# Performance work log

Hardware: AMD Instinct MI355X
Metric: run time of the kernel (lower is better)

Reference implementation:

```python
import jax, jax.numpy as jnp
import numpy as np

C = 512
H = 8
P = 64
B = 4
N = 1024


def setup_inputs() -> dict:
    key = jax.random.key(0)
    ks = jax.random.split(key, 12)
    s = 0.02
    return {
        "tokens": jax.random.normal(ks[0], (B, N, C), dtype=jnp.float32),
        "pair_features": jax.random.normal(ks[1], (N, N, P), dtype=jnp.float32),
        "Wq": jax.random.normal(ks[2], (C, C), dtype=jnp.float32) * s,
        "bq": jnp.zeros((C,), dtype=jnp.float32),
        "Wk": jax.random.normal(ks[3], (C, C), dtype=jnp.float32) * s,
        "bk": jnp.zeros((C,), dtype=jnp.float32),
        "Wv": jax.random.normal(ks[4], (C, C), dtype=jnp.float32) * s,
        "bv": jnp.zeros((C,), dtype=jnp.float32),
        "Wo": jax.random.normal(ks[5], (C, C), dtype=jnp.float32) * s,
        "bo": jnp.zeros((C,), dtype=jnp.float32),
        "Wp": jax.random.normal(ks[6], (P, H), dtype=jnp.float32) * s,
    }


def reference(tokens, pair_features, Wq, bq, Wk, bk, Wv, bv, Wo, bo, Wp):
    b, n, c = tokens.shape
    h = H
    d = c // h
    scale = d ** -0.5
    # projections -> [b, h, n, d]
    q = (tokens @ Wq + bq).reshape(b, n, h, d).transpose(0, 2, 1, 3)
    k = (tokens @ Wk + bk).reshape(b, n, h, d).transpose(0, 2, 1, 3)
    v = (tokens @ Wv + bv).reshape(b, n, h, d).transpose(0, 2, 1, 3)
    # attention logits [b, h, n, n] with additive pair-derived bias [h, n, n]
    logits = jnp.einsum('bhnd,bhmd->bhnm', q, k) * scale
    pair_bias = jnp.einsum('nmp,ph->hnm', pair_features, Wp)
    logits = logits + pair_bias[None]
    attn = jax.nn.softmax(logits, axis=-1)  # dropout p=0.0 -> identity
    merged = jnp.einsum('bhnm,bhmd->bhnd', attn, v)
    merged = merged.transpose(0, 2, 1, 3).reshape(b, n, c)
    return merged @ Wo + bo
```

## Files before the change

kernel.cpp:

```cpp
#include <hip/hip_runtime.h>
#include <hip/hip_bf16.h>
#include <stdint.h>
#include <stddef.h>

typedef __bf16 bf16x8 __attribute__((ext_vector_type(8)));
typedef __bf16 bf16x4 __attribute__((ext_vector_type(4)));
typedef float  f32x4  __attribute__((ext_vector_type(4)));
typedef uint32_t __attribute__((address_space(3))) lds_u32;
typedef uint32_t __attribute__((address_space(1))) glob_u32;

#define PAIR_BLOCKS 2048
#define CAST_BLOCKS 2048
#define TR_BLOCKS   256
#define NSPLIT 2
#define NITER  8
#define LOG2E 1.4426950408889634f

__global__ __launch_bounds__(256) void prep_kernel(
    const float* __restrict__ tokens, const float* __restrict__ pf,
    const float* __restrict__ Wq, const float* __restrict__ Wk,
    const float* __restrict__ Wv, const float* __restrict__ Wo,
    const float* __restrict__ Wp,
    __bf16* __restrict__ tok_bf, __bf16* __restrict__ WcatT,
    __bf16* __restrict__ WoT, __bf16* __restrict__ pbb) {
  __shared__ float ls[64][65];
  int bx = blockIdx.x, tid = threadIdx.x;
  if (bx < PAIR_BLOCKS) {
    int wave = tid >> 6, lane = tid & 63;
    int lg = lane >> 4, lr = lane & 15;
    bf16x8 whi[2], wlo[2];
#pragma unroll
    for (int s = 0; s < 2; ++s)
#pragma unroll
      for (int j = 0; j < 8; ++j) {
        int p = s * 32 + lg * 8 + j;
        float w = (lr < 8) ? Wp[p * 8 + lr] : 0.f;
        __bf16 h = (__bf16)w;
        whi[s][j] = h;
        wlo[s][j] = (__bf16)(w - (float)h);
      }
    int wbase = bx * 512 + wave * 128;
#pragma unroll 2
    for (int t = 0; t < 8; ++t) {
      int rowt = wbase + t * 16;
      const float* rp = pf + (size_t)(rowt + lr) * 64;
      f32x4 raw[2][2];
#pragma unroll
      for (int s = 0; s < 2; ++s) {
        raw[s][0] = *(const f32x4*)&rp[s * 32 + lg * 8];
        raw[s][1] = *(const f32x4*)&rp[s * 32 + lg * 8 + 4];
      }
      bf16x8 ahi[2], alo[2];
#pragma unroll
      for (int s = 0; s < 2; ++s)
#pragma unroll
        for (int j = 0; j < 8; ++j) {
          float x = raw[s][j >> 2][j & 3];
          __bf16 h = (__bf16)x;
          ahi[s][j] = h;
          alo[s][j] = (__bf16)(x - (float)h);
        }
      f32x4 acc = {0.f, 0.f, 0.f, 0.f};
#pragma unroll
      for (int s = 0; s < 2; ++s) {
        acc = __builtin_amdgcn_mfma_f32_16x16x32_bf16(ahi[s], whi[s], acc, 0, 0, 0);
        acc = __builtin_amdgcn_mfma_f32_16x16x32_bf16(ahi[s], wlo[s], acc, 0, 0, 0);
        acc = __builtin_amdgcn_mfma_f32_16x16x32_bf16(alo[s], whi[s], acc, 0, 0, 0);
      }
      if (lr < 8) {
        bf16x4 pk;
#pragma unroll
        for (int r = 0; r < 4; ++r) pk[r] = (__bf16)(acc[r] * LOG2E);
        *(bf16x4*)&pbb[((size_t)lr << 20) + rowt + lg * 4] = pk;
      }
    }
  } else if (bx < PAIR_BLOCKS + CAST_BLOCKS) {
    int i = (bx - PAIR_BLOCKS) * 256 + tid;
    float4 f = ((const float4*)tokens)[i];
    bf16x4 v;
    v[0] = (__bf16)f.x; v[1] = (__bf16)f.y; v[2] = (__bf16)f.z; v[3] = (__bf16)f.w;
    ((bf16x4*)tok_bf)[i] = v;
  } else {
    int t = bx - (PAIR_BLOCKS + CAST_BLOCKS);
    int which = t >> 6; t &= 63;
    const float* in = which == 0 ? Wq : which == 1 ? Wk : which == 2 ? Wv : Wo;
    __bf16* out = which < 3 ? (WcatT + (size_t)which * 512 * 512) : WoT;
    int tc = (t & 7) * 64, tr = (t >> 3) * 64;
#pragma unroll
    for (int i = 0; i < 16; ++i) {
      int e = tid + i * 256, r = e >> 6, c = e & 63;
      ls[r][c] = in[(size_t)(tr + r) * 512 + tc + c];
    }
    __syncthreads();
#pragma unroll
    for (int i = 0; i < 16; ++i) {
      int e = tid + i * 256, r = e >> 6, c = e & 63;
      out[(size_t)(tc + r) * 512 + tr + c] = (__bf16)ls[c][r];
    }
  }
}

__device__ __forceinline__ void gemm_mainloop_128(const __bf16* __restrict__ A,
                                                  const __bf16* __restrict__ Bt,
                                                  int K, int m0, int n0,
                                                  f32x4 (&acc)[4][4]) {
  __shared__ __bf16 As[128][40];
  __shared__ __bf16 Bs[128][40];
  int tid = threadIdx.x;
  int wave = tid >> 6, lane = tid & 63;
  int wm = (wave >> 1) * 64, wn = (wave & 1) * 64;
  int lg = lane >> 4, lr = lane & 15;
#pragma unroll
  for (int i = 0; i < 4; ++i)
#pragma unroll
    for (int j = 0; j < 4; ++j) acc[i][j] = (f32x4){0.f, 0.f, 0.f, 0.f};

  for (int k0 = 0; k0 < K; k0 += 32) {
    __syncthreads();
#pragma unroll
    for (int i = 0; i < 2; ++i) {
      int cid = tid + i * 256;
      int row = cid >> 2, c8 = (cid & 3) * 8;
      *(bf16x8*)&As[row][c8] = *(const bf16x8*)&A[(size_t)(m0 + row) * K + k0 + c8];
      *(bf16x8*)&Bs[row][c8] = *(const bf16x8*)&Bt[(size_t)(n0 + row) * K + k0 + c8];
    }
    __syncthreads();
    bf16x8 af[4], bfr[4];
#pragma unroll
    for (int i = 0; i < 4; ++i) {
      af[i]  = *(const bf16x8*)&As[wm + i * 16 + lr][lg * 8];
      bfr[i] = *(const bf16x8*)&Bs[wn + i * 16 + lr][lg * 8];
    }
#pragma unroll
    for (int i = 0; i < 4; ++i)
#pragma unroll
      for (int j = 0; j < 4; ++j)
        acc[i][j] = __builtin_amdgcn_mfma_f32_16x16x32_bf16(af[i], bfr[j], acc[i][j], 0, 0, 0);
  }
}

__global__ __launch_bounds__(256) void qkv_gemm_kernel(const __bf16* __restrict__ A,
                                                       const __bf16* __restrict__ Bt,
                                                       const float* __restrict__ bq,
                                                       const float* __restrict__ bk,
                                                       const float* __restrict__ bv,
                                                       __bf16* __restrict__ qb,
                                                       __bf16* __restrict__ kb,
                                                       __bf16* __restrict__ vtb) {
  const float qscale = 0.125f * LOG2E;
  int m0 = blockIdx.y * 128, n0 = blockIdx.x * 128;
  f32x4 acc[4][4];
  gemm_mainloop_128(A, Bt, 512, m0, n0, acc);
  int tid = threadIdx.x, wave = tid >> 6, lane = tid & 63;
  int wm = (wave >> 1) * 64, wn = (wave & 1) * 64, lg = lane >> 4, lr = lane & 15;
#pragma unroll
  for (int i = 0; i < 4; ++i)
#pragma unroll
    for (int j = 0; j < 4; ++j) {
      int grow0 = m0 + wm + i * 16 + lg * 4;
      int gcol = n0 + wn + j * 16 + lr;
      int sel = gcol >> 9, c = gcol & 511;
      int hh = c >> 6, dd = c & 63;
      int b = grow0 >> 10, n = grow0 & 1023;
      if (sel == 2) {
        float bias = bv[c];
        bf16x4 pack;
#pragma unroll
        for (int r = 0; r < 4; ++r) pack[r] = (__bf16)(acc[i][j][r] + bias);
        *(bf16x4*)&vtb[(((size_t)(b * 8 + hh)) * 64 + dd) * 1024 + n] = pack;
      } else if (sel == 0) {
        float bias = bq[c];
#pragma unroll
        for (int r = 0; r < 4; ++r)
          qb[(((size_t)(b * 8 + hh)) * 1024 + n + r) * 64 + dd] = (__bf16)((acc[i][j][r] + bias) * qscale);
      } else {
        float bias = bk[c];
#pragma unroll
        for (int r = 0; r < 4; ++r)
          kb[(((size_t)(b * 8 + hh)) * 1024 + n + r) * 64 + dd] = (__bf16)(acc[i][j][r] + bias);
      }
    }
}

__device__ __forceinline__ bf16x8 swz_read(const __bf16* buf, int r, int k) {
  int chunk = (r << 3) | (k ^ (r & 7));
  return *(const bf16x8*)&buf[chunk * 8];
}

__global__ __launch_bounds__(256) void flash_kernel(const __bf16* __restrict__ qg,
                                                    const __bf16* __restrict__ kg,
                                                    const __bf16* __restrict__ vtg,
                                                    const __bf16* __restrict__ pbg,
                                                    float* __restrict__ po,
                                                    float2* __restrict__ ml) {
  __shared__ __align__(16) __bf16 kvs[2][2][64 * 64];
  __shared__ __bf16 pls[4][16][72];
  int bh = blockIdx.y, z = blockIdx.z, h = bh & 7;
  int q0 = blockIdx.x * 64;
  int tid = threadIdx.x, wave = tid >> 6, lane = tid & 63;
  int lg = lane >> 4, lr = lane & 15;
  const __bf16* qp = qg + (size_t)bh * 65536;
  const __bf16* kp = kg + (size_t)bh * 65536;
  const __bf16* vp = vtg + (size_t)bh * 65536;
  const __bf16* pbh = pbg + ((size_t)h << 20);
  int qw0 = q0 + wave * 16;
  int kb0 = z * NITER;

  auto stage = [&](int buf, int kb2) {
#pragma unroll
    for (int p = 0; p < 2; ++p) {
      int c = p * 256 + wave * 64 + lane;
      int r = c >> 3, kk = c & 7;
      int g = (c & ~7) | (kk ^ (r & 7));
      const __bf16* gk = kp + (size_t)kb2 * 4096 + g * 8;
      const __bf16* gv = vp + (size_t)(g >> 3) * 1024 + kb2 * 64 + (g & 7) * 8;
      __builtin_amdgcn_global_load_lds((const glob_u32*)gk,
          (lds_u32*)&kvs[buf][0][(size_t)(p * 256 + wave * 64) * 8], 16, 0, 0);
      __builtin_amdgcn_global_load_lds((const glob_u32*)gv,
          (lds_u32*)&kvs[buf][1][(size_t)(p * 256 + wave * 64) * 8], 16, 0, 0);
    }
  };

  bf16x8 qf[2];
#pragma unroll
  for (int c = 0; c < 2; ++c)
    qf[c] = *(const bf16x8*)&qp[(size_t)(qw0 + lr) * 64 + c * 32 + lg * 8];

  float mrow = -1e30f, lrow = 0.f;
  f32x4 of[4] = {};

  stage(0, kb0);
  __syncthreads();

#pragma unroll
  for (int t = 0; t < NITER; ++t) {
    int kb2 = kb0 + t;
    if (t + 1 < NITER) stage((t + 1) & 1, kb2 + 1);
    const __bf16* kbuf = &kvs[t & 1][0][0];
    const __bf16* vbuf = &kvs[t & 1][1][0];

    bf16x8 kf[4][2];
#pragma unroll
    for (int n = 0; n < 4; ++n)
#pragma unroll
      for (int c = 0; c < 2; ++c)
        kf[n][c] = swz_read(kbuf, n * 16 + lr, c * 4 + lg);

    f32x4 sv[4];
#pragma unroll
    for (int n = 0; n < 4; ++n) {
      bf16x4 bias = *(const bf16x4*)&pbh[(size_t)(qw0 + lr) * 1024 + kb2 * 64 + n * 16 + lg * 4];
      f32x4 cb;
#pragma unroll
      for (int r = 0; r < 4; ++r) cb[r] = (float)bias[r];
      cb = __builtin_amdgcn_mfma_f32_16x16x32_bf16(kf[n][0], qf[0], cb, 0, 0, 0);
      cb = __builtin_amdgcn_mfma_f32_16x16x32_bf16(kf[n][1], qf[1], cb, 0, 0, 0);
      sv[n] = cb;
    }

    float tm = -1e30f;
#pragma unroll
    for (int n = 0; n < 4; ++n)
#pragma unroll
      for (int r = 0; r < 4; ++r) tm = fmaxf(tm, sv[n][r]);
    tm = fmaxf(tm, __shfl_xor(tm, 16));
    tm = fmaxf(tm, __shfl_xor(tm, 32));
    float newm = fmaxf(mrow, tm);
    float fs = exp2f(mrow - newm);
    mrow = newm;
    float rs = 0.f;
#pragma unroll
    for (int n = 0; n < 4; ++n)
#pragma unroll
      for (int r = 0; r < 4; ++r) {
        float p = exp2f(sv[n][r] - newm);
        sv[n][r] = p;
        rs += p;
      }
    rs += __shfl_xor(rs, 16);
    rs += __shfl_xor(rs, 32);
    lrow = lrow * fs + rs;

#pragma unroll
    for (int n = 0; n < 4; ++n) {
      bf16x4 pk;
#pragma unroll
      for (int r = 0; r < 4; ++r) pk[r] = (__bf16)sv[n][r];
      *(bf16x4*)&pls[wave][lr][n * 16 + lg * 4] = pk;
    }

#pragma unroll
    for (int r = 0; r < 4; ++r) {
      float fsq = __shfl(fs, (lane & 48) | (lg * 4 + r));
#pragma unroll
      for (int dn = 0; dn < 4; ++dn) of[dn][r] *= fsq;
    }

    bf16x8 pa[2];
#pragma unroll
    for (int c = 0; c < 2; ++c)
      pa[c] = *(const bf16x8*)&pls[wave][lr][c * 32 + lg * 8];
    bf16x8 vf[4][2];
#pragma unroll
    for (int dn = 0; dn < 4; ++dn)
#pragma unroll
      for (int c = 0; c < 2; ++c)
        vf[dn][c] = swz_read(vbuf, dn * 16 + lr, c * 4 + lg);
#pragma unroll
    for (int dn = 0; dn < 4; ++dn) {
      of[dn] = __builtin_amdgcn_mfma_f32_16x16x32_bf16(pa[0], vf[dn][0], of[dn], 0, 0, 0);
      of[dn] = __builtin_amdgcn_mfma_f32_16x16x32_bf16(pa[1], vf[dn][1], of[dn], 0, 0, 0);
    }
    __syncthreads();
  }

  if (lg == 0)
    ml[(size_t)z * 32768 + bh * 1024 + qw0 + lr] = make_float2(mrow, lrow);
#pragma unroll
  for (int r = 0; r < 4; ++r) {
    int q = qw0 + lg * 4 + r;
#pragma unroll
    for (int dn = 0; dn < 4; ++dn)
      po[((size_t)z * 32768 + bh * 1024 + q) * 64 + dn * 16 + lr] = of[dn][r];
  }
}

__global__ __launch_bounds__(256) void combine_kernel(const float* __restrict__ po,
                                                      const float2* __restrict__ ml,
                                                      __bf16* __restrict__ merged) {
  int e = blockIdx.x * 256 + threadIdx.x;
  int row = e >> 5, d2 = (e & 31) * 2;
  int bh = row >> 10, q = row & 1023, b = bh >> 3, h = bh & 7;
  float2 s[NSPLIT];
  float M = -1e30f;
#pragma unroll
  for (int zz = 0; zz < NSPLIT; ++zz) {
    s[zz] = ml[(size_t)zz * 32768 + row];
    M = fmaxf(M, s[zz].x);
  }
  float L = 0.f, ox = 0.f, oy = 0.f;
#pragma unroll
  for (int zz = 0; zz < NSPLIT; ++zz) {
    float w = exp2f(s[zz].x - M);
    L += w * s[zz].y;
    float2 p = *(const float2*)&po[((size_t)zz * 32768 + row) * 64 + d2];
    ox += w * p.x;
    oy += w * p.y;
  }
  float inv = 1.f / L;
  __bf16 pr[2] = {(__bf16)(ox * inv), (__bf16)(oy * inv)};
  *(uint32_t*)&merged[((size_t)(b * 1024 + q)) * 512 + h * 64 + d2] = *(uint32_t*)pr;
}

__global__ __launch_bounds__(256) void out_gemm_kernel(const __bf16* __restrict__ A,
                                                       const __bf16* __restrict__ Bt,
                                                       const float* __restrict__ bo,
                                                       float* __restrict__ out) {
  int m0 = blockIdx.y * 128, n0 = blockIdx.x * 128;
  f32x4 acc[4][4];
  gemm_mainloop_128(A, Bt, 512, m0, n0, acc);
  int tid = threadIdx.x, wave = tid >> 6, lane = tid & 63;
  int wm = (wave >> 1) * 64, wn = (wave & 1) * 64, lg = lane >> 4, lr = lane & 15;
#pragma unroll
  for (int i = 0; i < 4; ++i)
#pragma unroll
    for (int j = 0; j < 4; ++j)
#pragma unroll
      for (int r = 0; r < 4; ++r) {
        int grow = m0 + wm + i * 16 + lg * 4 + r;
        int gcol = n0 + wn + j * 16 + lr;
        out[(size_t)grow * 512 + gcol] = acc[i][j][r] + bo[gcol];
      }
}

extern "C" void kernel_launch(void* const* d_in, const int* in_sizes, int n_in,
                              void* d_out, int out_size, void* d_ws, size_t ws_size,
                              hipStream_t stream) {
  const float* tokens = (const float*)d_in[0];
  const float* pf     = (const float*)d_in[1];
  const float* Wq     = (const float*)d_in[2];
  const float* bq     = (const float*)d_in[3];
  const float* Wk     = (const float*)d_in[4];
  const float* bk     = (const float*)d_in[5];
  const float* Wv     = (const float*)d_in[6];
  const float* bv     = (const float*)d_in[7];
  const float* Wo     = (const float*)d_in[8];
  const float* bo     = (const float*)d_in[9];
  const float* Wp     = (const float*)d_in[10];
  float* out = (float*)d_out;

  char* ws = (char*)d_ws;
  size_t off = 0;
  auto alloc = [&](size_t bytes) { char* p = ws + off; off += (bytes + 255) & ~(size_t)255; return p; };
  __bf16* tok_bf = (__bf16*)alloc((size_t)4096 * 512 * 2);
  __bf16* WcatT  = (__bf16*)alloc((size_t)1536 * 512 * 2);
  __bf16* WoT    = (__bf16*)alloc((size_t)512 * 512 * 2);
  __bf16* qb     = (__bf16*)alloc((size_t)32 * 1024 * 64 * 2);
  __bf16* kb     = (__bf16*)alloc((size_t)32 * 1024 * 64 * 2);
  __bf16* vtb    = (__bf16*)alloc((size_t)32 * 64 * 1024 * 2);
  __bf16* pbb    = (__bf16*)alloc((size_t)8 * 1024 * 1024 * 2);
  __bf16* merged = (__bf16*)alloc((size_t)4096 * 512 * 2);
  float*  po     = (float*)alloc((size_t)NSPLIT * 32 * 1024 * 64 * 4);
  float2* ml     = (float2*)alloc((size_t)NSPLIT * 32 * 1024 * 8);

  prep_kernel<<<PAIR_BLOCKS + CAST_BLOCKS + TR_BLOCKS, 256, 0, stream>>>(
      tokens, pf, Wq, Wk, Wv, Wo, Wp, tok_bf, WcatT, WoT, pbb);
  qkv_gemm_kernel<<<dim3(12, 32), 256, 0, stream>>>(tok_bf, WcatT, bq, bk, bv, qb, kb, vtb);
  flash_kernel<<<dim3(16, 32, NSPLIT), 256, 0, stream>>>(qb, kb, vtb, pbb, po, ml);
  combine_kernel<<<4096, 256, 0, stream>>>(po, ml, merged);
  out_gemm_kernel<<<dim3(4, 32), 256, 0, stream>>>(merged, WoT, bo, out);
}
```

Baseline: 142.5 us.

## Fuse weight cast into GEMMs, merge prep with QKV, fold split combine into flash

The separate token/weight bf16 cast and transpose pass is removed. The QKV and output GEMMs now load fp32 tokens and weights directly and convert and transpose them in LDS. The QKV GEMM runs as extra blocks inside the pair-bias prep kernel, and the split-K combine is done by whichever flash block finishes last for each tile, using an atomic counter. This cuts the launch count from five to three and avoids workspace round-trips, at the cost of redundant fp32 weight conversion per block, more LDS per block, and a reliance on threadfence/atomic ordering.

```diff
diff --git a/kernel.cpp b/kernel.cpp
--- a/kernel.cpp
+++ b/kernel.cpp
@@ -9,23 +9,113 @@
 typedef uint32_t __attribute__((address_space(3))) lds_u32;
 typedef uint32_t __attribute__((address_space(1))) glob_u32;
 
+#define QKV_BLOCKS 384
 #define PAIR_BLOCKS 2048
-#define CAST_BLOCKS 2048
-#define TR_BLOCKS   256
+#define FLAG_BLOCKS 2
 #define NSPLIT 2
 #define NITER  8
 #define LOG2E 1.4426950408889634f
 
-__global__ __launch_bounds__(256) void prep_kernel(
+__global__ __launch_bounds__(256) void k1_kernel(
     const float* __restrict__ tokens, const float* __restrict__ pf,
     const float* __restrict__ Wq, const float* __restrict__ Wk,
-    const float* __restrict__ Wv, const float* __restrict__ Wo,
-    const float* __restrict__ Wp,
-    __bf16* __restrict__ tok_bf, __bf16* __restrict__ WcatT,
-    __bf16* __restrict__ WoT, __bf16* __restrict__ pbb) {
-  __shared__ float ls[64][65];
+    const float* __restrict__ Wv, const float* __restrict__ Wp,
+    const float* __restrict__ bq, const float* __restrict__ bk,
+    const float* __restrict__ bv,
+    __bf16* __restrict__ qb, __bf16* __restrict__ kb, __bf16* __restrict__ vtb,
+    __bf16* __restrict__ pbb, int* __restrict__ flag) {
+  __shared__ __bf16 As[128][40];
+  __shared__ __bf16 Bs[128][40];
+  __shared__ float ftile[32][133];
   int bx = blockIdx.x, tid = threadIdx.x;
-  if (bx < PAIR_BLOCKS) {
+  if (bx < QKV_BLOCKS) {
+    const float qscale = 0.125f * LOG2E;
+    int nb = bx % 12, mb = bx / 12;
+    int m0 = mb * 128, n0 = nb * 128;
+    int sel = n0 >> 9, cloc = n0 & 511;
+    const float* W = sel == 0 ? Wq : sel == 1 ? Wk : Wv;
+    int wave = tid >> 6, lane = tid & 63;
+    int wm = (wave >> 1) * 64, wn = (wave & 1) * 64;
+    int lg = lane >> 4, lr = lane & 15;
+    f32x4 acc[4][4];
+#pragma unroll
+    for (int i = 0; i < 4; ++i)
+#pragma unroll
+      for (int j = 0; j < 4; ++j) acc[i][j] = (f32x4){0.f, 0.f, 0.f, 0.f};
+
+    for (int k0 = 0; k0 < 512; k0 += 32) {
+      __syncthreads();
+#pragma unroll
+      for (int i = 0; i < 2; ++i) {
+        int cid = tid + i * 256;
+        int row = cid >> 2, c8 = (cid & 3) * 8;
+        const float* src = &tokens[(size_t)(m0 + row) * 512 + k0 + c8];
+        f32x4 f0 = *(const f32x4*)src, f1 = *(const f32x4*)(src + 4);
+        bf16x8 v;
+#pragma unroll
+        for (int u = 0; u < 4; ++u) { v[u] = (__bf16)f0[u]; v[u + 4] = (__bf16)f1[u]; }
+        *(bf16x8*)&As[row][c8] = v;
+      }
+#pragma unroll
+      for (int i = 0; i < 2; ++i) {
+        int cid = tid + i * 256;
+        int kk = cid >> 4, n8 = (cid & 15) * 8;
+        const float* src = &W[(size_t)(k0 + kk) * 512 + cloc + n8];
+        *(f32x4*)&ftile[kk][n8] = *(const f32x4*)src;
+        *(f32x4*)&ftile[kk][n8 + 4] = *(const f32x4*)(src + 4);
+      }
+      __syncthreads();
+#pragma unroll
+      for (int i = 0; i < 2; ++i) {
+        int cid = tid + i * 256;
+        int n = cid >> 2, kk8 = (cid & 3) * 8;
+        bf16x8 v;
+#pragma unroll
+        for (int u = 0; u < 8; ++u) v[u] = (__bf16)ftile[kk8 + u][n];
+        *(bf16x8*)&Bs[n][kk8] = v;
+      }
+      __syncthreads();
+      bf16x8 af[4], bfr[4];
+#pragma unroll
+      for (int i = 0; i < 4; ++i) {
+        af[i]  = *(const bf16x8*)&As[wm + i * 16 + lr][lg * 8];
+        bfr[i] = *(const bf16x8*)&Bs[wn + i * 16 + lr][lg * 8];
+      }
+#pragma unroll
+      for (int i = 0; i < 4; ++i)
+#pragma unroll
+        for (int j = 0; j < 4; ++j)
+          acc[i][j] = __builtin_amdgcn_mfma_f32_16x16x32_bf16(af[i], bfr[j], acc[i][j], 0, 0, 0);
+    }
+#pragma unroll
+    for (int i = 0; i < 4; ++i)
+#pragma unroll
+      for (int j = 0; j < 4; ++j) {
+        int grow0 = m0 + wm + i * 16 + lg * 4;
+        int gcol = n0 + wn + j * 16 + lr;
+        int gsel = gcol >> 9, c = gcol & 511;
+        int hh = c >> 6, dd = c & 63;
+        int b = grow0 >> 10, n = grow0 & 1023;
+        if (gsel == 2) {
+          float bias = bv[c];
+          bf16x4 pack;
+#pragma unroll
+          for (int r = 0; r < 4; ++r) pack[r] = (__bf16)(acc[i][j][r] + bias);
+          *(bf16x4*)&vtb[(((size_t)(b * 8 + hh)) * 64 + dd) * 1024 + n] = pack;
+        } else if (gsel == 0) {
+          float bias = bq[c];
+#pragma unroll
+          for (int r = 0; r < 4; ++r)
+            qb[(((size_t)(b * 8 + hh)) * 1024 + n + r) * 64 + dd] = (__bf16)((acc[i][j][r] + bias) * qscale);
+        } else {
+          float bias = bk[c];
+#pragma unroll
+          for (int r = 0; r < 4; ++r)
+            kb[(((size_t)(b * 8 + hh)) * 1024 + n + r) * 64 + dd] = (__bf16)(acc[i][j][r] + bias);
+        }
+      }
+  } else if (bx < QKV_BLOCKS + PAIR_BLOCKS) {
+    int pb = bx - QKV_BLOCKS;
     int wave = tid >> 6, lane = tid & 63;
     int lg = lane >> 4, lr = lane & 15;
     bf16x8 whi[2], wlo[2];
@@ -39,7 +129,7 @@
         whi[s][j] = h;
         wlo[s][j] = (__bf16)(w - (float)h);
       }
-    int wbase = bx * 512 + wave * 128;
+    int wbase = pb * 512 + wave * 128;
 #pragma unroll 2
     for (int t = 0; t < 8; ++t) {
       int rowt = wbase + t * 16;
@@ -74,112 +164,10 @@
         *(bf16x4*)&pbb[((size_t)lr << 20) + rowt + lg * 4] = pk;
       }
     }
-  } else if (bx < PAIR_BLOCKS + CAST_BLOCKS) {
-    int i = (bx - PAIR_BLOCKS) * 256 + tid;
-    float4 f = ((const float4*)tokens)[i];
-    bf16x4 v;
-    v[0] = (__bf16)f.x; v[1] = (__bf16)f.y; v[2] = (__bf16)f.z; v[3] = (__bf16)f.w;
-    ((bf16x4*)tok_bf)[i] = v;
   } else {
-    int t = bx - (PAIR_BLOCKS + CAST_BLOCKS);
-    int which = t >> 6; t &= 63;
-    const float* in = which == 0 ? Wq : which == 1 ? Wk : which == 2 ? Wv : Wo;
-    __bf16* out = which < 3 ? (WcatT + (size_t)which * 512 * 512) : WoT;
-    int tc = (t & 7) * 64, tr = (t >> 3) * 64;
-#pragma unroll
-    for (int i = 0; i < 16; ++i) {
-      int e = tid + i * 256, r = e >> 6, c = e & 63;
-      ls[r][c] = in[(size_t)(tr + r) * 512 + tc + c];
-    }
-    __syncthreads();
-#pragma unroll
-    for (int i = 0; i < 16; ++i) {
-      int e = tid + i * 256, r = e >> 6, c = e & 63;
-      out[(size_t)(tc + r) * 512 + tr + c] = (__bf16)ls[c][r];
-    }
-  }
-}
-
-__device__ __forceinline__ void gemm_mainloop_128(const __bf16* __restrict__ A,
-                                                  const __bf16* __restrict__ Bt,
-                                                  int K, int m0, int n0,
-                                                  f32x4 (&acc)[4][4]) {
-  __shared__ __bf16 As[128][40];
-  __shared__ __bf16 Bs[128][40];
-  int tid = threadIdx.x;
-  int wave = tid >> 6, lane = tid & 63;
-  int wm = (wave >> 1) * 64, wn = (wave & 1) * 64;
-  int lg = lane >> 4, lr = lane & 15;
-#pragma unroll
-  for (int i = 0; i < 4; ++i)
-#pragma unroll
-    for (int j = 0; j < 4; ++j) acc[i][j] = (f32x4){0.f, 0.f, 0.f, 0.f};
-
-  for (int k0 = 0; k0 < K; k0 += 32) {
-    __syncthreads();
-#pragma unroll
-    for (int i = 0; i < 2; ++i) {
-      int cid = tid + i * 256;
-      int row = cid >> 2, c8 = (cid & 3) * 8;
-      *(bf16x8*)&As[row][c8] = *(const bf16x8*)&A[(size_t)(m0 + row) * K + k0 + c8];
-      *(bf16x8*)&Bs[row][c8] = *(const bf16x8*)&Bt[(size_t)(n0 + row) * K + k0 + c8];
-    }
-    __syncthreads();
-    bf16x8 af[4], bfr[4];
-#pragma unroll
-    for (int i = 0; i < 4; ++i) {
-      af[i]  = *(const bf16x8*)&As[wm + i * 16 + lr][lg * 8];
-      bfr[i] = *(const bf16x8*)&Bs[wn + i * 16 + lr][lg * 8];
-    }
-#pragma unroll
-    for (int i = 0; i < 4; ++i)
-#pragma unroll
-      for (int j = 0; j < 4; ++j)
-        acc[i][j] = __builtin_amdgcn_mfma_f32_16x16x32_bf16(af[i], bfr[j], acc[i][j], 0, 0, 0);
-  }
-}
-
-__global__ __launch_bounds__(256) void qkv_gemm_kernel(const __bf16* __restrict__ A,
-                                                       const __bf16* __restrict__ Bt,
-                                                       const float* __restrict__ bq,
-                                                       const float* __restrict__ bk,
-                                                       const float* __restrict__ bv,
-                                                       __bf16* __restrict__ qb,
-                                                       __bf16* __restrict__ kb,
-                                                       __bf16* __restrict__ vtb) {
-  const float qscale = 0.125f * LOG2E;
-  int m0 = blockIdx.y * 128, n0 = blockIdx.x * 128;
-  f32x4 acc[4][4];
-  gemm_mainloop_128(A, Bt, 512, m0, n0, acc);
-  int tid = threadIdx.x, wave = tid >> 6, lane = tid & 63;
-  int wm = (wave >> 1) * 64, wn = (wave & 1) * 64, lg = lane >> 4, lr = lane & 15;
-#pragma unroll
-  for (int i = 0; i < 4; ++i)
-#pragma unroll
-    for (int j = 0; j < 4; ++j) {
-      int grow0 = m0 + wm + i * 16 + lg * 4;
-      int gcol = n0 + wn + j * 16 + lr;
-      int sel = gcol >> 9, c = gcol & 511;
-      int hh = c >> 6, dd = c & 63;
-      int b = grow0 >> 10, n = grow0 & 1023;
-      if (sel == 2) {
-        float bias = bv[c];
-        bf16x4 pack;
-#pragma unroll
-        for (int r = 0; r < 4; ++r) pack[r] = (__bf16)(acc[i][j][r] + bias);
-        *(bf16x4*)&vtb[(((size_t)(b * 8 + hh)) * 64 + dd) * 1024 + n] = pack;
-      } else if (sel == 0) {
-        float bias = bq[c];
-#pragma unroll
-        for (int r = 0; r < 4; ++r)
-          qb[(((size_t)(b * 8 + hh)) * 1024 + n + r) * 64 + dd] = (__bf16)((acc[i][j][r] + bias) * qscale);
-      } else {
-        float bias = bk[c];
-#pragma unroll
-        for (int r = 0; r < 4; ++r)
-          kb[(((size_t)(b * 8 + hh)) * 1024 + n + r) * 64 + dd] = (__bf16)(acc[i][j][r] + bias);
-      }
-    }
+    int idx = (bx - QKV_BLOCKS - PAIR_BLOCKS) * 256 + tid;
+    if (idx < 512) flag[idx] = 0;
+  }
 }
 
 __device__ __forceinline__ bf16x8 swz_read(const __bf16* buf, int r, int k) {
@@ -192,9 +180,12 @@
                                                     const __bf16* __restrict__ vtg,
                                                     const __bf16* __restrict__ pbg,
                                                     float* __restrict__ po,
-                                                    float2* __restrict__ ml) {
+                                                    float2* __restrict__ ml,
+                                                    int* __restrict__ flag,
+                                                    __bf16* __restrict__ merged) {
   __shared__ __align__(16) __bf16 kvs[2][2][64 * 64];
   __shared__ __bf16 pls[4][16][72];
+  __shared__ int winner;
   int bh = blockIdx.y, z = blockIdx.z, h = bh & 7;
   int q0 = blockIdx.x * 64;
   int tid = threadIdx.x, wave = tid >> 6, lane = tid & 63;
@@ -323,44 +314,89 @@
     for (int dn = 0; dn < 4; ++dn)
       po[((size_t)z * 32768 + bh * 1024 + q) * 64 + dn * 16 + lr] = of[dn][r];
   }
+
+  __syncthreads();
+  if (tid == 0) {
+    __threadfence();
+    winner = atomicAdd(&flag[blockIdx.x * 32 + bh], 1);
+  }
+  __syncthreads();
+  if (winner == NSPLIT - 1) {
+    __threadfence();
+    int r = tid >> 2, dseg = (tid & 3) * 16;
+    int rowg = bh * 1024 + q0 + r;
+    float2 s0 = ml[rowg], s1 = ml[32768 + rowg];
+    float M = fmaxf(s0.x, s1.x);
+    float w0 = exp2f(s0.x - M), w1 = exp2f(s1.x - M);
+    float inv = 1.f / (w0 * s0.y + w1 * s1.y);
+    const float* p0 = &po[(size_t)rowg * 64 + dseg];
+    const float* p1 = &po[(size_t)(32768 + rowg) * 64 + dseg];
+    __bf16 tmp[16];
+#pragma unroll
+    for (int u = 0; u < 16; ++u)
+      tmp[u] = (__bf16)((w0 * p0[u] + w1 * p1[u]) * inv);
+    int b = bh >> 3;
+    size_t base = ((size_t)(b * 1024 + q0 + r)) * 512 + h * 64 + dseg;
+    *(bf16x8*)&merged[base] = *(bf16x8*)&tmp[0];
+    *(bf16x8*)&merged[base + 8] = *(bf16x8*)&tmp[8];
+  }
 }
 
-__global__ __launch_bounds__(256) void combine_kernel(const float* __restrict__ po,
-                                                      const float2* __restrict__ ml,
-                                                      __bf16* __restrict__ merged) {
-  int e = blockIdx.x * 256 + threadIdx.x;
-  int row = e >> 5, d2 = (e & 31) * 2;
-  int bh = row >> 10, q = row & 1023, b = bh >> 3, h = bh & 7;
-  float2 s[NSPLIT];
-  float M = -1e30f;
-#pragma unroll
-  for (int zz = 0; zz < NSPLIT; ++zz) {
-    s[zz] = ml[(size_t)zz * 32768 + row];
-    M = fmaxf(M, s[zz].x);
-  }
-  float L = 0.f, ox = 0.f, oy = 0.f;
-#pragma unroll
-  for (int zz = 0; zz < NSPLIT; ++zz) {
-    float w = exp2f(s[zz].x - M);
-    L += w * s[zz].y;
-    float2 p = *(const float2*)&po[((size_t)zz * 32768 + row) * 64 + d2];
-    ox += w * p.x;
-    oy += w * p.y;
-  }
-  float inv = 1.f / L;
-  __bf16 pr[2] = {(__bf16)(ox * inv), (__bf16)(oy * inv)};
-  *(uint32_t*)&merged[((size_t)(b * 1024 + q)) * 512 + h * 64 + d2] = *(uint32_t*)pr;
-}
-
 __global__ __launch_bounds__(256) void out_gemm_kernel(const __bf16* __restrict__ A,
-                                                       const __bf16* __restrict__ Bt,
+                                                       const float* __restrict__ Wo,
                                                        const float* __restrict__ bo,
                                                        float* __restrict__ out) {
+  __shared__ __bf16 As[128][40];
+  __shared__ __bf16 Bs[128][40];
+  __shared__ float ftile[32][133];
   int m0 = blockIdx.y * 128, n0 = blockIdx.x * 128;
-  f32x4 acc[4][4];
-  gemm_mainloop_128(A, Bt, 512, m0, n0, acc);
   int tid = threadIdx.x, wave = tid >> 6, lane = tid & 63;
   int wm = (wave >> 1) * 64, wn = (wave & 1) * 64, lg = lane >> 4, lr = lane & 15;
+  f32x4 acc[4][4];
+#pragma unroll
+  for (int i = 0; i < 4; ++i)
+#pragma unroll
+    for (int j = 0; j < 4; ++j) acc[i][j] = (f32x4){0.f, 0.f, 0.f, 0.f};
+
+  for (int k0 = 0; k0 < 512; k0 += 32) {
+    __syncthreads();
+#pragma unroll
+    for (int i = 0; i < 2; ++i) {
+      int cid = tid + i * 256;
+      int row = cid >> 2, c8 = (cid & 3) * 8;
+      *(bf16x8*)&As[row][c8] = *(const bf16x8*)&A[(size_t)(m0 + row) * 512 + k0 + c8];
+    }
+#pragma unroll
+    for (int i = 0; i < 2; ++i) {
+      int cid = tid + i * 256;
+      int kk = cid >> 4, n8 = (cid & 15) * 8;
+      const float* src = &Wo[(size_t)(k0 + kk) * 512 + n0 + n8];
+      *(f32x4*)&ftile[kk][n8] = *(const f32x4*)src;
+      *(f32x4*)&ftile[kk][n8 + 4] = *(const f32x4*)(src + 4);
+    }
+    __syncthreads();
+#pragma unroll
+    for (int i = 0; i < 2; ++i) {
+      int cid = tid + i * 256;
+      int n = cid >> 2, kk8 = (cid & 3) * 8;
+      bf16x8 v;
+#pragma unroll
+      for (int u = 0; u < 8; ++u) v[u] = (__bf16)ftile[kk8 + u][n];
+      *(bf16x8*)&Bs[n][kk8] = v;
+    }
+    __syncthreads();
+    bf16x8 af[4], bfr[4];
+#pragma unroll
+    for (int i = 0; i < 4; ++i) {
+      af[i]  = *(const bf16x8*)&As[wm + i * 16 + lr][lg * 8];
+      bfr[i] = *(const bf16x8*)&Bs[wn + i * 16 + lr][lg * 8];
+    }
+#pragma unroll
+    for (int i = 0; i < 4; ++i)
+#pragma unroll
+      for (int j = 0; j < 4; ++j)
+        acc[i][j] = __builtin_amdgcn_mfma_f32_16x16x32_bf16(af[i], bfr[j], acc[i][j], 0, 0, 0);
+  }
 #pragma unroll
   for (int i = 0; i < 4; ++i)
 #pragma unroll
@@ -392,9 +428,6 @@
   char* ws = (char*)d_ws;
   size_t off = 0;
   auto alloc = [&](size_t bytes) { char* p = ws + off; off += (bytes + 255) & ~(size_t)255; return p; };
-  __bf16* tok_bf = (__bf16*)alloc((size_t)4096 * 512 * 2);
-  __bf16* WcatT  = (__bf16*)alloc((size_t)1536 * 512 * 2);
-  __bf16* WoT    = (__bf16*)alloc((size_t)512 * 512 * 2);
   __bf16* qb     = (__bf16*)alloc((size_t)32 * 1024 * 64 * 2);
   __bf16* kb     = (__bf16*)alloc((size_t)32 * 1024 * 64 * 2);
   __bf16* vtb    = (__bf16*)alloc((size_t)32 * 64 * 1024 * 2);
@@ -402,11 +435,10 @@
   __bf16* merged = (__bf16*)alloc((size_t)4096 * 512 * 2);
   float*  po     = (float*)alloc((size_t)NSPLIT * 32 * 1024 * 64 * 4);
   float2* ml     = (float2*)alloc((size_t)NSPLIT * 32 * 1024 * 8);
-
-  prep_kernel<<<PAIR_BLOCKS + CAST_BLOCKS + TR_BLOCKS, 256, 0, stream>>>(
-      tokens, pf, Wq, Wk, Wv, Wo, Wp, tok_bf, WcatT, WoT, pbb);
-  qkv_gemm_kernel<<<dim3(12, 32), 256, 0, stream>>>(tok_bf, WcatT, bq, bk, bv, qb, kb, vtb);
-  flash_kernel<<<dim3(16, 32, NSPLIT), 256, 0, stream>>>(qb, kb, vtb, pbb, po, ml);
-  combine_kernel<<<4096, 256, 0, stream>>>(po, ml, merged);
-  out_gemm_kernel<<<dim3(4, 32), 256, 0, stream>>>(merged, WoT, bo, out);
+  int*    flag   = (int*)alloc(512 * 4);
+
+  k1_kernel<<<QKV_BLOCKS + PAIR_BLOCKS + FLAG_BLOCKS, 256, 0, stream>>>(
+      tokens, pf, Wq, Wk, Wv, Wp, bq, bk, bv, qb, kb, vtb, pbb, flag);
+  flash_kernel<<<dim3(16, 32, NSPLIT), 256, 0, stream>>>(qb, kb, vtb, pbb, po, ml, flag, merged);
+  out_gemm_kernel<<<dim3(4, 32), 256, 0, stream>>>(merged, Wo, bo, out);
 }
```

New measurement: 223.4 us. 56.8% more time.

## Fuse split-K combine into flash kernel and simplify pair-bias projection

Applied to the files above, without the earlier changes.

The separate combine kernel is removed. The second-finishing flash block for each (query tile, head) now merges the two partial results through an atomic counter that prep_kernel resets, which saves a launch and a pass over the partial outputs. The pair-bias projection also drops the hi/lo bf16 split compensation, going from three MFMAs per k-slice to one. It now stages pair features through swizzled LDS so the global loads are coalesced. The cost is lower precision in the pair bias and reliance on threadfence/atomic ordering for correctness.

```diff
diff --git a/kernel.cpp b/kernel.cpp
--- a/kernel.cpp
+++ b/kernel.cpp
@@ -22,51 +22,51 @@
     const float* __restrict__ Wv, const float* __restrict__ Wo,
     const float* __restrict__ Wp,
     __bf16* __restrict__ tok_bf, __bf16* __restrict__ WcatT,
-    __bf16* __restrict__ WoT, __bf16* __restrict__ pbb) {
-  __shared__ float ls[64][65];
+    __bf16* __restrict__ WoT, __bf16* __restrict__ pbb, int* __restrict__ flag) {
+  __shared__ __align__(16) float smem[64 * 65];
   int bx = blockIdx.x, tid = threadIdx.x;
   if (bx < PAIR_BLOCKS) {
     int wave = tid >> 6, lane = tid & 63;
     int lg = lane >> 4, lr = lane & 15;
-    bf16x8 whi[2], wlo[2];
+    bf16x8 wfrag[2];
 #pragma unroll
     for (int s = 0; s < 2; ++s)
 #pragma unroll
       for (int j = 0; j < 8; ++j) {
         int p = s * 32 + lg * 8 + j;
-        float w = (lr < 8) ? Wp[p * 8 + lr] : 0.f;
-        __bf16 h = (__bf16)w;
-        whi[s][j] = h;
-        wlo[s][j] = (__bf16)(w - (float)h);
-      }
+        wfrag[s][j] = (lr < 8) ? (__bf16)Wp[p * 8 + lr] : (__bf16)0.f;
+      }
+    char* psbase = (char*)smem + wave * 4096;
     int wbase = bx * 512 + wave * 128;
+    int wrow_lo = lane >> 4;
+    int wcol = lane & 15;
 #pragma unroll 2
-    for (int t = 0; t < 8; ++t) {
-      int rowt = wbase + t * 16;
-      const float* rp = pf + (size_t)(rowt + lr) * 64;
-      f32x4 raw[2][2];
+    for (int it = 0; it < 8; ++it) {
+      int rowt = wbase + it * 16;
+      const float* base = pf + (size_t)rowt * 64;
+      f32x4 v[4];
+#pragma unroll
+      for (int j = 0; j < 4; ++j)
+        v[j] = *(const f32x4*)(base + j * 256 + lane * 4);
+      char* ps = psbase + (it & 1) * 2048;
+#pragma unroll
+      for (int j = 0; j < 4; ++j) {
+        int jr = j * 4 + wrow_lo;
+        bf16x4 b;
+#pragma unroll
+        for (int u = 0; u < 4; ++u) b[u] = (__bf16)v[j][u];
+        int cbyte = ((((wcol >> 1) ^ (jr & 7)) << 4) | ((wcol & 1) << 3));
+        *(bf16x4*)(ps + jr * 128 + cbyte) = b;
+      }
+      bf16x8 af[2];
 #pragma unroll
       for (int s = 0; s < 2; ++s) {
-        raw[s][0] = *(const f32x4*)&rp[s * 32 + lg * 8];
-        raw[s][1] = *(const f32x4*)&rp[s * 32 + lg * 8 + 4];
-      }
-      bf16x8 ahi[2], alo[2];
-#pragma unroll
-      for (int s = 0; s < 2; ++s)
-#pragma unroll
-        for (int j = 0; j < 8; ++j) {
-          float x = raw[s][j >> 2][j & 3];
-          __bf16 h = (__bf16)x;
-          ahi[s][j] = h;
-          alo[s][j] = (__bf16)(x - (float)h);
-        }
+        int cb = ((s * 4 + lg) ^ (lr & 7)) << 4;
+        af[s] = *(const bf16x8*)(ps + lr * 128 + cb);
+      }
       f32x4 acc = {0.f, 0.f, 0.f, 0.f};
-#pragma unroll
-      for (int s = 0; s < 2; ++s) {
-        acc = __builtin_amdgcn_mfma_f32_16x16x32_bf16(ahi[s], whi[s], acc, 0, 0, 0);
-        acc = __builtin_amdgcn_mfma_f32_16x16x32_bf16(ahi[s], wlo[s], acc, 0, 0, 0);
-        acc = __builtin_amdgcn_mfma_f32_16x16x32_bf16(alo[s], whi[s], acc, 0, 0, 0);
-      }
+      acc = __builtin_amdgcn_mfma_f32_16x16x32_bf16(af[0], wfrag[0], acc, 0, 0, 0);
+      acc = __builtin_amdgcn_mfma_f32_16x16x32_bf16(af[1], wfrag[1], acc, 0, 0, 0);
       if (lr < 8) {
         bf16x4 pk;
 #pragma unroll
@@ -80,11 +80,12 @@
     bf16x4 v;
     v[0] = (__bf16)f.x; v[1] = (__bf16)f.y; v[2] = (__bf16)f.z; v[3] = (__bf16)f.w;
     ((bf16x4*)tok_bf)[i] = v;
-  } else {
+  } else if (bx < PAIR_BLOCKS + CAST_BLOCKS + TR_BLOCKS) {
     int t = bx - (PAIR_BLOCKS + CAST_BLOCKS);
     int which = t >> 6; t &= 63;
     const float* in = which == 0 ? Wq : which == 1 ? Wk : which == 2 ? Wv : Wo;
     __bf16* out = which < 3 ? (WcatT + (size_t)which * 512 * 512) : WoT;
+    float (*ls)[65] = (float(*)[65])smem;
     int tc = (t & 7) * 64, tr = (t >> 3) * 64;
 #pragma unroll
     for (int i = 0; i < 16; ++i) {
@@ -97,6 +98,9 @@
       int e = tid + i * 256, r = e >> 6, c = e & 63;
       out[(size_t)(tc + r) * 512 + tr + c] = (__bf16)ls[c][r];
     }
+  } else {
+    flag[tid] = 0;
+    flag[tid + 256] = 0;
   }
 }
 
@@ -192,9 +196,12 @@
                                                     const __bf16* __restrict__ vtg,
                                                     const __bf16* __restrict__ pbg,
                                                     float* __restrict__ po,
-                                                    float2* __restrict__ ml) {
+                                                    float2* __restrict__ ml,
+                                                    int* __restrict__ flag,
+                                                    __bf16* __restrict__ merged) {
   __shared__ __align__(16) __bf16 kvs[2][2][64 * 64];
   __shared__ __bf16 pls[4][16][72];
+  __shared__ int winner;
   int bh = blockIdx.y, z = blockIdx.z, h = bh & 7;
   int q0 = blockIdx.x * 64;
   int tid = threadIdx.x, wave = tid >> 6, lane = tid & 63;
@@ -323,33 +330,32 @@
     for (int dn = 0; dn < 4; ++dn)
       po[((size_t)z * 32768 + bh * 1024 + q) * 64 + dn * 16 + lr] = of[dn][r];
   }
-}
-
-__global__ __launch_bounds__(256) void combine_kernel(const float* __restrict__ po,
-                                                      const float2* __restrict__ ml,
-                                                      __bf16* __restrict__ merged) {
-  int e = blockIdx.x * 256 + threadIdx.x;
-  int row = e >> 5, d2 = (e & 31) * 2;
-  int bh = row >> 10, q = row & 1023, b = bh >> 3, h = bh & 7;
-  float2 s[NSPLIT];
-  float M = -1e30f;
-#pragma unroll
-  for (int zz = 0; zz < NSPLIT; ++zz) {
-    s[zz] = ml[(size_t)zz * 32768 + row];
-    M = fmaxf(M, s[zz].x);
-  }
-  float L = 0.f, ox = 0.f, oy = 0.f;
-#pragma unroll
-  for (int zz = 0; zz < NSPLIT; ++zz) {
-    float w = exp2f(s[zz].x - M);
-    L += w * s[zz].y;
-    float2 p = *(const float2*)&po[((size_t)zz * 32768 + row) * 64 + d2];
-    ox += w * p.x;
-    oy += w * p.y;
-  }
-  float inv = 1.f / L;
-  __bf16 pr[2] = {(__bf16)(ox * inv), (__bf16)(oy * inv)};
-  *(uint32_t*)&merged[((size_t)(b * 1024 + q)) * 512 + h * 64 + d2] = *(uint32_t*)pr;
+
+  __syncthreads();
+  if (tid == 0) {
+    __threadfence();
+    winner = atomicAdd(&flag[blockIdx.x * 32 + bh], 1);
+  }
+  __syncthreads();
+  if (winner == NSPLIT - 1) {
+    __threadfence();
+    int r = tid >> 2, dseg = (tid & 3) * 16;
+    int rowg = bh * 1024 + q0 + r;
+    float2 s0 = ml[rowg], s1 = ml[32768 + rowg];
+    float M = fmaxf(s0.x, s1.x);
+    float w0 = exp2f(s0.x - M), w1 = exp2f(s1.x - M);
+    float inv = 1.f / (w0 * s0.y + w1 * s1.y);
+    const float* p0 = &po[(size_t)rowg * 64 + dseg];
+    const float* p1 = &po[(size_t)(32768 + rowg) * 64 + dseg];
+    __bf16 tmp[16];
+#pragma unroll
+    for (int u = 0; u < 16; ++u)
+      tmp[u] = (__bf16)((w0 * p0[u] + w1 * p1[u]) * inv);
+    int b = bh >> 3;
+    size_t base = ((size_t)(b * 1024 + q0 + r)) * 512 + h * 64 + dseg;
+    *(bf16x8*)&merged[base] = *(bf16x8*)&tmp[0];
+    *(bf16x8*)&merged[base + 8] = *(bf16x8*)&tmp[8];
+  }
 }
 
 __global__ __launch_bounds__(256) void out_gemm_kernel(const __bf16* __restrict__ A,
@@ -402,11 +408,11 @@
   __bf16* merged = (__bf16*)alloc((size_t)4096 * 512 * 2);
   float*  po     = (float*)alloc((size_t)NSPLIT * 32 * 1024 * 64 * 4);
   float2* ml     = (float2*)alloc((size_t)NSPLIT * 32 * 1024 * 8);
-
-  prep_kernel<<<PAIR_BLOCKS + CAST_BLOCKS + TR_BLOCKS, 256, 0, stream>>>(
-      tokens, pf, Wq, Wk, Wv, Wo, Wp, tok_bf, WcatT, WoT, pbb);
+  int*    flag   = (int*)alloc(512 * 4);
+
+  prep_kernel<<<PAIR_BLOCKS + CAST_BLOCKS + TR_BLOCKS + 1, 256, 0, stream>>>(
+      tokens, pf, Wq, Wk, Wv, Wo, Wp, tok_bf, WcatT, WoT, pbb, flag);
   qkv_gemm_kernel<<<dim3(12, 32), 256, 0, stream>>>(tok_bf, WcatT, bq, bk, bv, qb, kb, vtb);
-  flash_kernel<<<dim3(16, 32, NSPLIT), 256, 0, stream>>>(qb, kb, vtb, pbb, po, ml);
-  combine_kernel<<<4096, 256, 0, stream>>>(po, ml, merged);
+  flash_kernel<<<dim3(16, 32, NSPLIT), 256, 0, stream>>>(qb, kb, vtb, pbb, po, ml, flag, merged);
   out_gemm_kernel<<<dim3(4, 32), 256, 0, stream>>>(merged, WoT, bo, out);
 }
```

Result: slower. 225.3 us (+58.2%).
